# Kernel tuning notes

Measured on AMD Instinct MI355X. Metric: run time of the kernel, lower is better.

Reference implementation:

```python
import jax, jax.numpy as jnp
import numpy as np

EPS = 1e-5

def _ln(x, g=None, b=None):
    m = jnp.mean(x, axis=-1, keepdims=True)
    v = jnp.var(x, axis=-1, keepdims=True)
    y = (x - m) / jnp.sqrt(v + EPS)
    if g is not None:
        y = y * g + b
    return y

def setup_inputs() -> dict:
    key = jax.random.key(0)
    B, N, C = 2, 2048, 1024   # batch, tokens, query_dim
    H, D = 16, 64             # heads, dim_head -> inner = 1024
    inner = H * D
    ks = jax.random.split(key, 8)
    s = C ** -0.5
    inp = {
        'x':   jax.random.normal(ks[0], (B, N, C), jnp.float32),
        'w_q': jax.random.normal(ks[1], (C, inner), jnp.float32) * s,
        'b_q': jnp.zeros((inner,), jnp.float32),
        'w_k': jax.random.normal(ks[2], (C, inner), jnp.float32) * s,
        'b_k': jnp.zeros((inner,), jnp.float32),
        'w_v': jax.random.normal(ks[3], (C, inner), jnp.float32) * s,
        'b_v': jnp.zeros((inner,), jnp.float32),
        'g_q': jnp.ones((inner,), jnp.float32),
        'be_q': jnp.zeros((inner,), jnp.float32),
        'g_k': jnp.ones((inner,), jnp.float32),
        'be_k': jnp.zeros((inner,), jnp.float32),
        # to_out is zero-initialized in the torch code; use small random weights
        # so forward/backward are non-trivial for correctness testing.
        'w_o': jax.random.normal(ks[4], (inner, C), jnp.float32) * s,
        'b_o': jnp.zeros((C,), jnp.float32),
    }
    return inp

def reference(x, w_q, b_q, w_k, b_k, w_v, b_v, g_q, be_q, g_k, be_k, w_o, b_o):
    B, N, C = x.shape
    inner = w_q.shape[1]
    H = 16
    D = inner // H
    xn = _ln(x)                                  # pre-norm, no affine
    ctx = xn                                     # self-attention (context=None)
    silu = jax.nn.silu
    q = silu(xn) @ w_q + b_q                     # [B,N,inner]
    k = silu(ctx) @ w_k + b_k
    v = silu(ctx) @ w_v + b_v
    q = _ln(q, g_q, be_q)
    k = _ln(k, g_k, be_k)
    q = q * (inner ** -0.5)                      # NB: scale by inner_dim, pre-split
    q = q.reshape(B, N, H, D)
    k = k.reshape(B, N, H, D)
    v = v.reshape(B, N, H, D)
    w = jnp.einsum('bihd,bjhd->bhij', q, k)      # [B,H,N,N]
    w = jax.nn.softmax(w, axis=-1)
    o = jnp.einsum('bhij,bjhd->bihd', w, v).reshape(B, N, inner)
    return silu(o) @ w_o + b_o
```

## Files before the change

### kernel.cpp

```cpp
#include <hip/hip_runtime.h>
#include <hip/hip_bf16.h>
#include <math.h>

#define LN_EPS 1e-5f

typedef __attribute__((ext_vector_type(8))) short bf16x8;
typedef __attribute__((ext_vector_type(8))) short short8;
typedef __attribute__((ext_vector_type(4))) float f32x4;
typedef unsigned short ushort_t;

__device__ __forceinline__ float silu_f(float x) {
    return x / (1.0f + __expf(-x));
}

__device__ __forceinline__ ushort_t f2bf(float f) {
    __hip_bfloat16 h = __float2bfloat16(f);
    return *reinterpret_cast<ushort_t*>(&h);
}

__device__ __forceinline__ float bf2f(ushort_t u) {
    __hip_bfloat16 h = *reinterpret_cast<__hip_bfloat16*>(&u);
    return __bfloat162float(h);
}

__device__ __forceinline__ unsigned pk2(float a, float b) {
    unsigned r;
    asm("v_cvt_pk_bf16_f32 %0, %1, %2" : "=v"(r) : "v"(a), "v"(b));
    return r;
}

__device__ __forceinline__ float fast_exp2(float x) {
#if defined(__has_builtin)
#if __has_builtin(__builtin_amdgcn_exp2f)
    return __builtin_amdgcn_exp2f(x);
#else
    return exp2f(x);
#endif
#else
    return exp2f(x);
#endif
}

__device__ __forceinline__ void gld16(const void* g, void* lds) {
    __builtin_amdgcn_global_load_lds(
        (const __attribute__((address_space(1))) unsigned int*)g,
        (__attribute__((address_space(3))) unsigned int*)lds, 16, 0, 0);
}

__device__ __forceinline__ float2 block_reduce2(float2 p, float2* sbuf) {
    #pragma unroll
    for (int off = 32; off > 0; off >>= 1) {
        p.x += __shfl_down(p.x, off, 64);
        p.y += __shfl_down(p.y, off, 64);
    }
    int lane = threadIdx.x & 63;
    int wid  = threadIdx.x >> 6;
    if (lane == 0) sbuf[wid] = p;
    __syncthreads();
    if (threadIdx.x == 0) {
        float2 r = sbuf[0];
        for (int i = 1; i < 4; ++i) { r.x += sbuf[i].x; r.y += sbuf[i].y; }
        sbuf[0] = r;
    }
    __syncthreads();
    return sbuf[0];
}

__global__ __launch_bounds__(256) void ln_silu_kernel(
    const float* __restrict__ x, ushort_t* __restrict__ out)
{
    __shared__ float2 sbuf[4];
    const int C = 1024;
    int row = blockIdx.x;
    const float4* xr = (const float4*)(x + (size_t)row * C);
    float4 v = xr[threadIdx.x];
    float2 p;
    p.x = v.x + v.y + v.z + v.w;
    p.y = v.x*v.x + v.y*v.y + v.z*v.z + v.w*v.w;
    float2 s = block_reduce2(p, sbuf);
    float mean = s.x / (float)C;
    float var  = s.y / (float)C - mean * mean;
    float rstd = rsqrtf(var + LN_EPS);
    ushort4 y;
    y.x = f2bf(silu_f((v.x - mean) * rstd));
    y.y = f2bf(silu_f((v.y - mean) * rstd));
    y.z = f2bf(silu_f((v.z - mean) * rstd));
    y.w = f2bf(silu_f((v.w - mean) * rstd));
    ((ushort4*)(out + (size_t)row * C))[threadIdx.x] = y;
}

__global__ __launch_bounds__(256) void ln_affine_bf16(
    ushort_t* __restrict__ qk0, ushort_t* __restrict__ qk1,
    const float* __restrict__ g0, const float* __restrict__ be0,
    const float* __restrict__ g1, const float* __restrict__ be1,
    float scale0, float scale1)
{
    __shared__ float2 sbuf[4];
    const int C = 1024;
    int which = blockIdx.y;
    ushort_t* q = which ? qk1 : qk0;
    const float* g  = which ? g1  : g0;
    const float* be = which ? be1 : be0;
    float scale = which ? scale1 : scale0;
    int row = blockIdx.x;
    ushort4 u = ((ushort4*)(q + (size_t)row * C))[threadIdx.x];
    float v0 = bf2f(u.x), v1 = bf2f(u.y), v2 = bf2f(u.z), v3 = bf2f(u.w);
    float2 p;
    p.x = v0 + v1 + v2 + v3;
    p.y = v0*v0 + v1*v1 + v2*v2 + v3*v3;
    float2 s = block_reduce2(p, sbuf);
    float mean = s.x / (float)C;
    float var  = s.y / (float)C - mean * mean;
    float rstd = rsqrtf(var + LN_EPS);
    float4 gv = ((const float4*)g)[threadIdx.x];
    float4 bv = ((const float4*)be)[threadIdx.x];
    ushort4 y;
    y.x = f2bf(((v0 - mean) * rstd * gv.x + bv.x) * scale);
    y.y = f2bf(((v1 - mean) * rstd * gv.y + bv.y) * scale);
    y.z = f2bf(((v2 - mean) * rstd * gv.z + bv.z) * scale);
    y.w = f2bf(((v3 - mean) * rstd * gv.w + bv.w) * scale);
    ((ushort4*)(q + (size_t)row * C))[threadIdx.x] = y;
}

struct W4 { const float* p[4]; };

__global__ __launch_bounds__(256) void transpose_w(W4 w, ushort_t* __restrict__ outbase)
{
    __shared__ float Ls[64][65];
    int z = blockIdx.z;
    const float* in = w.p[z];
    ushort_t* out = outbase + (size_t)z * 1024 * 1024;
    int r0 = blockIdx.y * 64, c0 = blockIdx.x * 64;
    int t = threadIdx.x, r = t >> 2, j = (t & 3) * 16;
    #pragma unroll
    for (int i = 0; i < 4; ++i) {
        float4 v = *(const float4*)(in + (size_t)(r0 + r) * 1024 + c0 + j + i * 4);
        Ls[r][j + i*4 + 0] = v.x;
        Ls[r][j + i*4 + 1] = v.y;
        Ls[r][j + i*4 + 2] = v.z;
        Ls[r][j + i*4 + 3] = v.w;
    }
    __syncthreads();
    __align__(16) ushort_t tmp[16];
    #pragma unroll
    for (int i = 0; i < 16; ++i) tmp[i] = f2bf(Ls[j + i][r]);
    ushort_t* op = out + (size_t)(c0 + r) * 1024 + r0 + j;
    *(short8*)(op)     = *(short8*)(tmp);
    *(short8*)(op + 8) = *(short8*)(tmp + 8);
}

template<int BM, bool OUT_BF16>
__global__ __launch_bounds__(256) void gemm_mfma(
    const ushort_t* __restrict__ A, const ushort_t* __restrict__ Bt0,
    const float* __restrict__ b0, const float* __restrict__ b1,
    const float* __restrict__ b2, void* __restrict__ out0,
    ushort_t* __restrict__ vt_out,
    int M, int N, int K)
{
    constexpr int BK = 64;
    constexpr int MI = BM / 32;
    constexpr int LOADS = BM / 32 + 4;
    __shared__ ushort_t Smem[2 * (BM + 128) * BK];
    ushort_t* As0 = Smem;
    ushort_t* Bs0 = Smem + BM * BK;
    ushort_t* As1 = Smem + (BM + 128) * BK;
    ushort_t* Bs1 = As1 + BM * BK;

    int z = blockIdx.z;
    const ushort_t* Bt = Bt0 + (size_t)z * N * K;
    const float* bias = (z == 0) ? b0 : (z == 1) ? b1 : b2;

    int t = threadIdx.x;
    int lane = t & 63, wv = t >> 6;
    int wr = wv >> 1, wc = wv & 1;
    int quad = lane >> 4, ln16 = lane & 15;

    int row0 = blockIdx.y * BM;
    int col0 = blockIdx.x * 128;

    const f32x4 zero4 = {0.f, 0.f, 0.f, 0.f};
    f32x4 acc[MI][4];
    #pragma unroll
    for (int i = 0; i < MI; ++i)
        #pragma unroll
        for (int j = 0; j < 4; ++j) acc[i][j] = zero4;

    auto stage = [&](ushort_t* AsB, ushort_t* BsB, int kt) {
        #pragma unroll
        for (int c = 0; c < BM / 32; ++c) {
            int idx = c * 256 + t;
            int r = idx >> 3, ch = idx & 7;
            int g = ch ^ (r & 7);
            gld16(A + (size_t)(row0 + r) * K + kt + g * 8,
                  AsB + (size_t)(c * 256 + wv * 64) * 8);
        }
        #pragma unroll
        for (int c = 0; c < 4; ++c) {
            int idx = c * 256 + t;
            int r = idx >> 3, ch = idx & 7;
            int g = ch ^ (r & 7);
            gld16(Bt + (size_t)(col0 + r) * K + kt + g * 8,
                  BsB + (size_t)(c * 256 + wv * 64) * 8);
        }
    };

    auto compute = [&](const ushort_t* AsB, const ushort_t* BsB) {
        #pragma unroll
        for (int s = 0; s < 2; ++s) {
            bf16x8 af[MI], bf[4];
            int g = s * 4 + quad;
            #pragma unroll
            for (int i = 0; i < MI; ++i) {
                int m = wr * (BM / 2) + i * 16 + ln16;
                af[i] = *(const bf16x8*)(AsB + (size_t)(m * 8 + (g ^ (m & 7))) * 8);
            }
            #pragma unroll
            for (int j = 0; j < 4; ++j) {
                int n = wc * 64 + j * 16 + ln16;
                bf[j] = *(const bf16x8*)(BsB + (size_t)(n * 8 + (g ^ (n & 7))) * 8);
            }
            __builtin_amdgcn_s_setprio(1);
            #pragma unroll
            for (int i = 0; i < MI; ++i)
                #pragma unroll
                for (int j = 0; j < 4; ++j)
                    acc[i][j] = __builtin_amdgcn_mfma_f32_16x16x32_bf16(
                        af[i], bf[j], acc[i][j], 0, 0, 0);
            __builtin_amdgcn_s_setprio(0);
        }
    };

    auto wait_prev = [&]() {
        if constexpr (BM == 128) asm volatile("s_waitcnt vmcnt(8)" ::: "memory");
        else                     asm volatile("s_waitcnt vmcnt(6)" ::: "memory");
    };

    const int NTk = K / BK;
    stage(As0, Bs0, 0);
    #pragma unroll 1
    for (int it = 0; it < NTk; it += 2) {
        stage(As1, Bs1, (it + 1) * BK);
        wait_prev();
        __builtin_amdgcn_s_barrier();
        __builtin_amdgcn_sched_barrier(0);
        compute(As0, Bs0);
        __builtin_amdgcn_sched_barrier(0);
        __builtin_amdgcn_s_barrier();

        if (it + 2 < NTk) {
            stage(As0, Bs0, (it + 2) * BK);
            wait_prev();
        } else {
            asm volatile("s_waitcnt vmcnt(0)" ::: "memory");
        }
        __builtin_amdgcn_s_barrier();
        __builtin_amdgcn_sched_barrier(0);
        compute(As1, Bs1);
        __builtin_amdgcn_sched_barrier(0);
        __builtin_amdgcn_s_barrier();
    }

    if (OUT_BF16 && z == 2 && BM == 128) {
        ushort_t* tb = Smem + wv * 4096;
        int tok0 = row0 + wr * 64;
        int chn0 = col0 + wc * 64;
        #pragma unroll
        for (int j = 0; j < 4; ++j) {
            int chl = j * 16 + ln16;
            float bv = bias[chn0 + chl];
            #pragma unroll
            for (int i = 0; i < MI; ++i) {
                uint2 uu;
                uu.x = pk2(acc[i][j][0] + bv, acc[i][j][1] + bv);
                uu.y = pk2(acc[i][j][2] + bv, acc[i][j][3] + bv);
                int hc = i * 4 + quad;
                int phys = hc ^ ((chl & 7) << 1);
                *(uint2*)(tb + chl * 64 + phys * 4) = uu;
            }
        }
        int bb2 = tok0 >> 11;
        int tokb = tok0 & 2047;
        #pragma unroll
        for (int p = 0; p < 8; ++p) {
            int chl = p * 8 + (lane >> 3);
            int tc  = lane & 7;
            int ptc = tc ^ (chl & 7);
            uint4 vvv = *(const uint4*)(tb + chl * 64 + ptc * 8);
            *(uint4*)(vt_out + ((size_t)bb2 * 1024 + chn0 + chl) * 2048 + tokb + tc * 8) = vvv;
        }
    } else {
        #pragma unroll
        for (int j = 0; j < 4; ++j) {
            int col = col0 + wc * 64 + j * 16 + ln16;
            float bv = bias[col];
            #pragma unroll
            for (int i = 0; i < MI; ++i) {
                int rowb = row0 + wr * (BM / 2) + i * 16 + quad * 4;
                #pragma unroll
                for (int r = 0; r < 4; ++r) {
                    float val = acc[i][j][r] + bv;
                    if (OUT_BF16) {
                        ushort_t* out = (ushort_t*)out0 + (size_t)z * M * N;
                        out[(size_t)(rowb + r) * N + col] = f2bf(val);
                    } else {
                        float* out = (float*)out0;
                        out[(size_t)(rowb + r) * N + col] = val;
                    }
                }
            }
        }
    }
}

__global__ __launch_bounds__(256, 4) void flash_mfma(
    const ushort_t* __restrict__ qb, const ushort_t* __restrict__ kb,
    const ushort_t* __restrict__ vT, ushort_t* __restrict__ ob)
{
    const int N = 2048, HD = 1024, D = 64, H = 16;
    const int KT = 64;
    const int NT = N / KT;
    __shared__ ushort_t Ks[2][64 * 64];
    __shared__ ushort_t Vs[2][64 * 64];

    int t = threadIdx.x, lane = t & 63, wv = t >> 6;
    int quad = lane >> 4, ln16 = lane & 15;
    int qt = blockIdx.x, h = blockIdx.y, b = blockIdx.z;

    size_t qk_base = (size_t)b * N * HD + (size_t)h * D;
    size_t vt_base = (size_t)(b * H + h) * D * N;

    bf16x8 qf[2];
    {
        const ushort_t* qp = qb + qk_base + (size_t)(qt * 64 + wv * 16 + ln16) * HD;
        qf[0] = *(const bf16x8*)(qp + quad * 8);
        qf[1] = *(const bf16x8*)(qp + 32 + quad * 8);
    }

    bf16x8 ones;
    #pragma unroll
    for (int i = 0; i < 8; ++i) ones[i] = (short)0x3F80;

    const f32x4 zero4 = {0.f, 0.f, 0.f, 0.f};
    f32x4 oacc[4];
    f32x4 lacc = zero4;
    #pragma unroll
    for (int j = 0; j < 4; ++j) oacc[j] = zero4;

    auto stage_K = [&](ushort_t* KsB, int kt) {
        #pragma unroll
        for (int c = 0; c < 2; ++c) {
            int idx = c * 256 + t;
            int r = idx >> 3, ch = idx & 7, g = ch ^ (r & 7);
            int pr = (r & ~31) | (((r >> 2) & 3) << 3) | (((r >> 4) & 1) << 2) | (r & 3);
            gld16(kb + qk_base + (size_t)(kt + pr) * HD + g * 8,
                  KsB + (size_t)(c * 256 + wv * 64) * 8);
        }
    };
    auto stage_V = [&](ushort_t* VsB, int kt) {
        #pragma unroll
        for (int c = 0; c < 2; ++c) {
            int idx = c * 256 + t;
            int r = idx >> 3, ch = idx & 7, g = ch ^ (r & 7);
            gld16(vT + vt_base + (size_t)r * N + kt + g * 8,
                  VsB + (size_t)(c * 256 + wv * 64) * 8);
        }
    };

    auto qk_tile = [&](const ushort_t* KsB, f32x4 (&st)[4]) {
        #pragma unroll
        for (int j = 0; j < 4; ++j) st[j] = zero4;
        __builtin_amdgcn_s_setprio(1);
        #pragma unroll
        for (int s = 0; s < 2; ++s) {
            int g = s * 4 + quad;
            #pragma unroll
            for (int j = 0; j < 4; ++j) {
                int n = j * 16 + ln16;
                bf16x8 kf = *(const bf16x8*)(KsB + ((size_t)n * 8 + (g ^ (n & 7))) * 8);
                st[j] = __builtin_amdgcn_mfma_f32_16x16x32_bf16(kf, qf[s], st[j], 0, 0, 0);
            }
        }
        __builtin_amdgcn_s_setprio(0);
    };

    auto sm_pv = [&](f32x4 (&st)[4], const ushort_t* VsB) {
        bf16x8 vf[2][4];
        #pragma unroll
        for (int w = 0; w < 2; ++w) {
            int phys = (w * 4 + quad) ^ (ln16 & 7);
            #pragma unroll
            for (int mt = 0; mt < 4; ++mt)
                vf[w][mt] = *(const bf16x8*)(VsB + (size_t)(mt * 16 + ln16) * 64 + phys * 8);
        }
        #pragma unroll
        for (int j = 0; j < 4; ++j) {
            st[j][0] = fast_exp2(st[j][0]);
            st[j][1] = fast_exp2(st[j][1]);
            st[j][2] = fast_exp2(st[j][2]);
            st[j][3] = fast_exp2(st[j][3]);
        }
        #pragma unroll
        for (int w = 0; w < 2; ++w) {
            uint4 up;
            up.x = pk2(st[2*w][0],   st[2*w][1]);
            up.y = pk2(st[2*w][2],   st[2*w][3]);
            up.z = pk2(st[2*w+1][0], st[2*w+1][1]);
            up.w = pk2(st[2*w+1][2], st[2*w+1][3]);
            bf16x8 pf = __builtin_bit_cast(bf16x8, up);
            __builtin_amdgcn_s_setprio(1);
            lacc = __builtin_amdgcn_mfma_f32_16x16x32_bf16(ones, pf, lacc, 0, 0, 0);
            #pragma unroll
            for (int mt = 0; mt < 4; ++mt)
                oacc[mt] = __builtin_amdgcn_mfma_f32_16x16x32_bf16(vf[w][mt], pf, oacc[mt], 0, 0, 0);
            __builtin_amdgcn_s_setprio(0);
        }
    };

    f32x4 stA[4], stB[4];

    stage_K(Ks[0], 0);       stage_V(Vs[0], 0);
    stage_K(Ks[1], KT);      stage_V(Vs[1], KT);
    asm volatile("s_waitcnt vmcnt(4)" ::: "memory");
    __builtin_amdgcn_s_barrier();
    __builtin_amdgcn_sched_barrier(0);
    qk_tile(Ks[0], stA);
    __builtin_amdgcn_sched_barrier(0);
    __builtin_amdgcn_s_barrier();

    #pragma unroll 1
    for (int it = 0; it < NT - 2; it += 2) {
        stage_K(Ks[0], (it + 2) * KT);
        asm volatile("s_waitcnt vmcnt(4)" ::: "memory");
        __builtin_amdgcn_s_barrier();
        __builtin_amdgcn_sched_barrier(0);
        qk_tile(Ks[1], stB);
        sm_pv(stA, Vs[0]);
        __builtin_amdgcn_sched_barrier(0);
        __builtin_amdgcn_s_barrier();
        stage_V(Vs[0], (it + 2) * KT);

        stage_K(Ks[1], (it + 3) * KT);
        asm volatile("s_waitcnt vmcnt(4)" ::: "memory");
        __builtin_amdgcn_s_barrier();
        __builtin_amdgcn_sched_barrier(0);
        qk_tile(Ks[0], stA);
        sm_pv(stB, Vs[1]);
        __builtin_amdgcn_sched_barrier(0);
        __builtin_amdgcn_s_barrier();
        stage_V(Vs[1], (it + 3) * KT);
    }

    asm volatile("s_waitcnt vmcnt(2)" ::: "memory");
    __builtin_amdgcn_s_barrier();
    __builtin_amdgcn_sched_barrier(0);
    qk_tile(Ks[1], stB);
    sm_pv(stA, Vs[0]);
    asm volatile("s_waitcnt vmcnt(0)" ::: "memory");
    __builtin_amdgcn_s_barrier();
    __builtin_amdgcn_sched_barrier(0);
    sm_pv(stB, Vs[1]);

    float inv = 1.0f / lacc[0];
    size_t rowoff = qk_base + (size_t)(qt * 64 + wv * 16 + ln16) * HD;
    #pragma unroll
    for (int mt = 0; mt < 4; ++mt) {
        float o0 = silu_f(oacc[mt][0] * inv);
        float o1 = silu_f(oacc[mt][1] * inv);
        float o2 = silu_f(oacc[mt][2] * inv);
        float o3 = silu_f(oacc[mt][3] * inv);
        uint2 uu;
        uu.x = pk2(o0, o1);
        uu.y = pk2(o2, o3);
        *(uint2*)(ob + rowoff + mt * 16 + quad * 4) = uu;
    }
}

extern "C" void kernel_launch(void* const* d_in, const int* in_sizes, int n_in,
                              void* d_out, int out_size, void* d_ws, size_t ws_size,
                              hipStream_t stream) {
    const float* x    = (const float*)d_in[0];
    const float* w_q  = (const float*)d_in[1];
    const float* b_q  = (const float*)d_in[2];
    const float* w_k  = (const float*)d_in[3];
    const float* b_k  = (const float*)d_in[4];
    const float* w_v  = (const float*)d_in[5];
    const float* b_v  = (const float*)d_in[6];
    const float* g_q  = (const float*)d_in[7];
    const float* be_q = (const float*)d_in[8];
    const float* g_k  = (const float*)d_in[9];
    const float* be_k = (const float*)d_in[10];
    const float* w_o  = (const float*)d_in[11];
    const float* b_o  = (const float*)d_in[12];
    float* out = (float*)d_out;

    const int B = 2, N = 2048, C = 1024, H = 16, INNER = 1024;
    const int M = B * N;
    const size_t MC = (size_t)M * C;

    ushort_t* ws  = (ushort_t*)d_ws;
    ushort_t* sx  = ws;
    ushort_t* qkv = ws + MC;
    ushort_t* vTp = ws + 4 * MC;
    ushort_t* wT  = ws + 5 * MC;

    ushort_t* qbuf = qkv;
    ushort_t* kbuf = qkv + MC;
    ushort_t* obuf = sx;

    W4 w4; w4.p[0] = w_q; w4.p[1] = w_k; w4.p[2] = w_v; w4.p[3] = w_o;
    transpose_w<<<dim3(16, 16, 4), 256, 0, stream>>>(w4, wT);

    ln_silu_kernel<<<M, 256, 0, stream>>>(x, sx);

    gemm_mfma<128, true><<<dim3(INNER / 128, M / 128, 3), 256, 0, stream>>>(
        sx, wT, b_q, b_k, b_v, qkv, vTp, M, INNER, C);

    ln_affine_bf16<<<dim3(M, 2), 256, 0, stream>>>(
        qbuf, kbuf, g_q, be_q, g_k, be_k, 0.03125f * 1.44269504f, 1.0f);

    flash_mfma<<<dim3(N / 64, H, B), 256, 0, stream>>>(qbuf, kbuf, vTp, obuf);

    gemm_mfma<64, false><<<dim3(C / 128, M / 64, 1), 256, 0, stream>>>(
        obuf, wT + (size_t)3 * 1024 * 1024, b_o, b_o, b_o, out, nullptr, M, C, INNER);
}
```

Baseline: 203.2 us.

## Split flash attention warps across query pairs and key halves with LDS reduction

Each wave now handles 32 query rows and half of each 64-key tile, in place of 16 query rows over the full tile. Every K and V fragment read from shared memory therefore feeds two MFMAs, which halves LDS fragment traffic per MFMA. The two key-half partial outputs and row sums are combined through shared memory at the end, reusing the K/V buffers. The cost is two extra barriers, an LDS reduction, more accumulator registers, and only half the waves doing the final normalise-and-store.

```diff
diff --git a/kernel.cpp b/kernel.cpp
--- a/kernel.cpp
+++ b/kernel.cpp
@@ -159,7 +159,6 @@
 {
     constexpr int BK = 64;
     constexpr int MI = BM / 32;
-    constexpr int LOADS = BM / 32 + 4;
     __shared__ ushort_t Smem[2 * (BM + 128) * BK];
     ushort_t* As0 = Smem;
     ushort_t* Bs0 = Smem + BM * BK;
@@ -324,16 +323,19 @@
 
     int t = threadIdx.x, lane = t & 63, wv = t >> 6;
     int quad = lane >> 4, ln16 = lane & 15;
+    int qh = wv & 1, kh = wv >> 1;
     int qt = blockIdx.x, h = blockIdx.y, b = blockIdx.z;
 
     size_t qk_base = (size_t)b * N * HD + (size_t)h * D;
     size_t vt_base = (size_t)(b * H + h) * D * N;
 
-    bf16x8 qf[2];
-    {
-        const ushort_t* qp = qb + qk_base + (size_t)(qt * 64 + wv * 16 + ln16) * HD;
-        qf[0] = *(const bf16x8*)(qp + quad * 8);
-        qf[1] = *(const bf16x8*)(qp + 32 + quad * 8);
+    bf16x8 qf[2][2];
+    #pragma unroll
+    for (int qg = 0; qg < 2; ++qg) {
+        const ushort_t* qp = qb + qk_base +
+            (size_t)(qt * 64 + qh * 32 + qg * 16 + ln16) * HD;
+        qf[qg][0] = *(const bf16x8*)(qp + quad * 8);
+        qf[qg][1] = *(const bf16x8*)(qp + 32 + quad * 8);
     }
 
     bf16x8 ones;
@@ -341,10 +343,14 @@
     for (int i = 0; i < 8; ++i) ones[i] = (short)0x3F80;
 
     const f32x4 zero4 = {0.f, 0.f, 0.f, 0.f};
-    f32x4 oacc[4];
-    f32x4 lacc = zero4;
-    #pragma unroll
-    for (int j = 0; j < 4; ++j) oacc[j] = zero4;
+    f32x4 oacc[2][4];
+    f32x4 lacc[2];
+    #pragma unroll
+    for (int qg = 0; qg < 2; ++qg) {
+        lacc[qg] = zero4;
+        #pragma unroll
+        for (int j = 0; j < 4; ++j) oacc[qg][j] = zero4;
+    }
 
     auto stage_K = [&](ushort_t* KsB, int kt) {
         #pragma unroll
@@ -366,57 +372,65 @@
         }
     };
 
-    auto qk_tile = [&](const ushort_t* KsB, f32x4 (&st)[4]) {
-        #pragma unroll
-        for (int j = 0; j < 4; ++j) st[j] = zero4;
+    auto qk_tile = [&](const ushort_t* KsB, f32x4 (&st)[2][2]) {
+        #pragma unroll
+        for (int u = 0; u < 2; ++u)
+            #pragma unroll
+            for (int qg = 0; qg < 2; ++qg) st[u][qg] = zero4;
         __builtin_amdgcn_s_setprio(1);
         #pragma unroll
         for (int s = 0; s < 2; ++s) {
             int g = s * 4 + quad;
             #pragma unroll
-            for (int j = 0; j < 4; ++j) {
-                int n = j * 16 + ln16;
+            for (int u = 0; u < 2; ++u) {
+                int n = (kh * 2 + u) * 16 + ln16;
                 bf16x8 kf = *(const bf16x8*)(KsB + ((size_t)n * 8 + (g ^ (n & 7))) * 8);
-                st[j] = __builtin_amdgcn_mfma_f32_16x16x32_bf16(kf, qf[s], st[j], 0, 0, 0);
+                st[u][0] = __builtin_amdgcn_mfma_f32_16x16x32_bf16(kf, qf[0][s], st[u][0], 0, 0, 0);
+                st[u][1] = __builtin_amdgcn_mfma_f32_16x16x32_bf16(kf, qf[1][s], st[u][1], 0, 0, 0);
             }
         }
         __builtin_amdgcn_s_setprio(0);
     };
 
-    auto sm_pv = [&](f32x4 (&st)[4], const ushort_t* VsB) {
-        bf16x8 vf[2][4];
-        #pragma unroll
-        for (int w = 0; w < 2; ++w) {
-            int phys = (w * 4 + quad) ^ (ln16 & 7);
+    auto sm_pv = [&](f32x4 (&st)[2][2], const ushort_t* VsB) {
+        bf16x8 vf[4];
+        {
+            int phys = (kh * 4 + quad) ^ (ln16 & 7);
             #pragma unroll
             for (int mt = 0; mt < 4; ++mt)
-                vf[w][mt] = *(const bf16x8*)(VsB + (size_t)(mt * 16 + ln16) * 64 + phys * 8);
-        }
-        #pragma unroll
-        for (int j = 0; j < 4; ++j) {
-            st[j][0] = fast_exp2(st[j][0]);
-            st[j][1] = fast_exp2(st[j][1]);
-            st[j][2] = fast_exp2(st[j][2]);
-            st[j][3] = fast_exp2(st[j][3]);
-        }
-        #pragma unroll
-        for (int w = 0; w < 2; ++w) {
+                vf[mt] = *(const bf16x8*)(VsB + (size_t)(mt * 16 + ln16) * 64 + phys * 8);
+        }
+        #pragma unroll
+        for (int u = 0; u < 2; ++u)
+            #pragma unroll
+            for (int qg = 0; qg < 2; ++qg) {
+                st[u][qg][0] = fast_exp2(st[u][qg][0]);
+                st[u][qg][1] = fast_exp2(st[u][qg][1]);
+                st[u][qg][2] = fast_exp2(st[u][qg][2]);
+                st[u][qg][3] = fast_exp2(st[u][qg][3]);
+            }
+        bf16x8 pf[2];
+        #pragma unroll
+        for (int qg = 0; qg < 2; ++qg) {
             uint4 up;
-            up.x = pk2(st[2*w][0],   st[2*w][1]);
-            up.y = pk2(st[2*w][2],   st[2*w][3]);
-            up.z = pk2(st[2*w+1][0], st[2*w+1][1]);
-            up.w = pk2(st[2*w+1][2], st[2*w+1][3]);
-            bf16x8 pf = __builtin_bit_cast(bf16x8, up);
-            __builtin_amdgcn_s_setprio(1);
-            lacc = __builtin_amdgcn_mfma_f32_16x16x32_bf16(ones, pf, lacc, 0, 0, 0);
-            #pragma unroll
-            for (int mt = 0; mt < 4; ++mt)
-                oacc[mt] = __builtin_amdgcn_mfma_f32_16x16x32_bf16(vf[w][mt], pf, oacc[mt], 0, 0, 0);
-            __builtin_amdgcn_s_setprio(0);
-        }
-    };
-
-    f32x4 stA[4], stB[4];
+            up.x = pk2(st[0][qg][0], st[0][qg][1]);
+            up.y = pk2(st[0][qg][2], st[0][qg][3]);
+            up.z = pk2(st[1][qg][0], st[1][qg][1]);
+            up.w = pk2(st[1][qg][2], st[1][qg][3]);
+            pf[qg] = __builtin_bit_cast(bf16x8, up);
+        }
+        __builtin_amdgcn_s_setprio(1);
+        lacc[0] = __builtin_amdgcn_mfma_f32_16x16x32_bf16(ones, pf[0], lacc[0], 0, 0, 0);
+        lacc[1] = __builtin_amdgcn_mfma_f32_16x16x32_bf16(ones, pf[1], lacc[1], 0, 0, 0);
+        #pragma unroll
+        for (int mt = 0; mt < 4; ++mt) {
+            oacc[0][mt] = __builtin_amdgcn_mfma_f32_16x16x32_bf16(vf[mt], pf[0], oacc[0][mt], 0, 0, 0);
+            oacc[1][mt] = __builtin_amdgcn_mfma_f32_16x16x32_bf16(vf[mt], pf[1], oacc[1][mt], 0, 0, 0);
+        }
+        __builtin_amdgcn_s_setprio(0);
+    };
+
+    f32x4 stA[2][2], stB[2][2];
 
     stage_K(Ks[0], 0);       stage_V(Vs[0], 0);
     stage_K(Ks[1], KT);      stage_V(Vs[1], KT);
@@ -460,18 +474,41 @@
     __builtin_amdgcn_sched_barrier(0);
     sm_pv(stB, Vs[1]);
 
-    float inv = 1.0f / lacc[0];
-    size_t rowoff = qk_base + (size_t)(qt * 64 + wv * 16 + ln16) * HD;
-    #pragma unroll
-    for (int mt = 0; mt < 4; ++mt) {
-        float o0 = silu_f(oacc[mt][0] * inv);
-        float o1 = silu_f(oacc[mt][1] * inv);
-        float o2 = silu_f(oacc[mt][2] * inv);
-        float o3 = silu_f(oacc[mt][3] * inv);
-        uint2 uu;
-        uu.x = pk2(o0, o1);
-        uu.y = pk2(o2, o3);
-        *(uint2*)(ob + rowoff + mt * 16 + quad * 4) = uu;
+    __syncthreads();
+    float* obufL = (float*)Ks;
+    float* lbufL = (float*)Vs;
+    if (kh == 1) {
+        float* base = obufL + qh * 2048;
+        #pragma unroll
+        for (int qg = 0; qg < 2; ++qg)
+            #pragma unroll
+            for (int mt = 0; mt < 4; ++mt)
+                *(f32x4*)(base + (qg * 4 + mt) * 256 + lane * 4) = oacc[qg][mt];
+        lbufL[qh * 128 + lane * 2 + 0] = lacc[0][0];
+        lbufL[qh * 128 + lane * 2 + 1] = lacc[1][0];
+    }
+    __syncthreads();
+    if (kh == 0) {
+        float* base = obufL + qh * 2048;
+        #pragma unroll
+        for (int qg = 0; qg < 2; ++qg) {
+            float l = lacc[qg][0] + lbufL[qh * 128 + lane * 2 + qg];
+            float inv = 1.0f / l;
+            size_t rowoff = qk_base +
+                (size_t)(qt * 64 + qh * 32 + qg * 16 + ln16) * HD;
+            #pragma unroll
+            for (int mt = 0; mt < 4; ++mt) {
+                f32x4 p = *(const f32x4*)(base + (qg * 4 + mt) * 256 + lane * 4);
+                float o0 = silu_f((oacc[qg][mt][0] + p[0]) * inv);
+                float o1 = silu_f((oacc[qg][mt][1] + p[1]) * inv);
+                float o2 = silu_f((oacc[qg][mt][2] + p[2]) * inv);
+                float o3 = silu_f((oacc[qg][mt][3] + p[3]) * inv);
+                uint2 uu;
+                uu.x = pk2(o0, o1);
+                uu.y = pk2(o2, o3);
+                *(uint2*)(ob + rowoff + mt * 16 + quad * 4) = uu;
+            }
+        }
     }
 }
 
```

Result: slower. 272.6 us (+34.1%).
